# Performance work log

Hardware: AMD Instinct MI355X
Metric: run time of the kernel (lower is better)

The kernel has to match this reference:

```python
import jax, jax.numpy as jnp
import numpy as np

HID = 1024
HEADS = 16

def setup_inputs() -> dict:
    key = jax.random.key(0)
    ks = jax.random.split(key, 9)
    s = 1.0 / np.sqrt(HID)
    x = jax.random.normal(ks[0], (4, 2048, HID), dtype=jnp.float32)
    Wq = jax.random.normal(ks[1], (HID, HID), dtype=jnp.float32) * s
    bq = jnp.zeros((HID,), dtype=jnp.float32)
    Wk = jax.random.normal(ks[2], (HID, HID), dtype=jnp.float32) * s
    bk = jnp.zeros((HID,), dtype=jnp.float32)
    Wv = jax.random.normal(ks[3], (HID, HID), dtype=jnp.float32) * s
    bv = jnp.zeros((HID,), dtype=jnp.float32)
    Wo = jax.random.normal(ks[4], (HID, HID), dtype=jnp.float32) * s
    bo = jnp.zeros((HID,), dtype=jnp.float32)
    return {"x": x, "Wq": Wq, "bq": bq, "Wk": Wk, "bk": bk,
            "Wv": Wv, "bv": bv, "Wo": Wo, "bo": bo}

def _split_heads(t):  # [b, n, hid] -> [b, h, n, d]
    b, n, _ = t.shape
    return t.reshape(b, n, HEADS, HID // HEADS).transpose(0, 2, 1, 3)

def reference(x, Wq, bq, Wk, bk, Wv, bv, Wo, bo):
    # nn.Linear: y = x @ W.T + b
    q = _split_heads(x @ Wq.T + bq)
    k = _split_heads(x @ Wk.T + bk)
    v = _split_heads(x @ Wv.T + bv)
    energy = jnp.einsum('bhqd,bhkd->bhqk', q, k)
    scaling = HID ** 0.5  # note: sqrt(hid_channels), NOT sqrt(head_dim)
    att = jax.nn.softmax(energy / scaling, axis=-1)
    out = jnp.einsum('bhqk,bhkd->bhqd', att, v)
    b, h, n, d = out.shape
    out = out.transpose(0, 2, 1, 3).reshape(b, n, h * d)
    return out @ Wo.T + bo
```

## Files before the change

### kernel.cpp

```cpp
#include <hip/hip_runtime.h>
#include <stdint.h>


#define HID 1024
#define NH 16
#define HD 64
#define BB 4
#define SEQ 2048
#define MTOT (BB * SEQ)

typedef short bf16x8 __attribute__((ext_vector_type(8)));
typedef float f32x4 __attribute__((ext_vector_type(4)));
typedef float f32x16 __attribute__((ext_vector_type(16)));

#define SWZ(row, cb) ((cb) ^ (((row) & 7) << 4))

#define GLDS(gp, lp) __builtin_amdgcn_global_load_lds( \
    (const __attribute__((address_space(1))) void*)(gp), \
    (__attribute__((address_space(3))) void*)(lp), 16, 0, 0)

static __device__ __forceinline__ unsigned short f2bf(float f) {
  unsigned u = __float_as_uint(f);
  u += 0x7fffu + ((u >> 16) & 1u);
  return (unsigned short)(u >> 16);
}

static __device__ __forceinline__ f32x4 mfma16(bf16x8 a, bf16x8 b, f32x4 c) {
  return __builtin_amdgcn_mfma_f32_16x16x32_bf16(a, b, c, 0, 0, 0);
}
static __device__ __forceinline__ f32x16 mfma32(bf16x8 a, bf16x8 b, f32x16 c) {
  return __builtin_amdgcn_mfma_f32_32x32x16_bf16(a, b, c, 0, 0, 0);
}

__global__ void k_cvt_all(const float* __restrict__ x,
                          const float* __restrict__ Wq, const float* __restrict__ Wk,
                          const float* __restrict__ Wv, const float* __restrict__ Wo,
                          unsigned short* __restrict__ ws) {
  const int X4 = MTOT * HID / 4;
  const int W4 = HID * HID / 4;
  int i = blockIdx.x * blockDim.x + threadIdx.x;
  const float* src;
  unsigned short* dst;
  int off;
  if (i < X4) {
    src = x; dst = ws; off = i;
  } else {
    int j = i - X4;
    int w = j / W4;
    off = j - w * W4;
    src = (w == 0) ? Wq : (w == 1) ? Wk : (w == 2) ? Wv : Wo;
    dst = ws + (size_t)MTOT * HID + (size_t)w * HID * HID;
  }
  float4 v = reinterpret_cast<const float4*>(src)[off];
  ushort4 o;
  o.x = f2bf(v.x); o.y = f2bf(v.y); o.z = f2bf(v.z); o.w = f2bf(v.w);
  reinterpret_cast<ushort4*>(dst)[off] = o;
}

__global__ __launch_bounds__(256, 2) void k_gemm3(
    const unsigned short* __restrict__ A,
    const unsigned short* __restrict__ W3,
    const float* __restrict__ bq, const float* __restrict__ bk,
    const float* __restrict__ bv,
    unsigned short* __restrict__ Qo,
    unsigned short* __restrict__ Ko,
    unsigned short* __restrict__ Vto,
    float cexp) {
  const int K = HID;
  __shared__ __align__(16) unsigned short sA[128 * 64];
  __shared__ __align__(16) unsigned short sB[128 * 64];
  const int orig = blockIdx.x + gridDim.x * blockIdx.y;
  const int xcd = orig & 7, idx = orig >> 3;
  const int gm = xcd & 3, gn = xcd >> 1 >> 1;
  const int m0 = (gm * 16 + (idx & 15)) * 128;
  const int n0 = (gn * 12 + (idx >> 4)) * 128;
  const int tid = threadIdx.x;
  const int lane = tid & 63, wid = tid >> 6;
  const int wr = wid >> 1, wc = wid & 1;
  const int lr = lane & 15, lg = lane >> 4;

  f32x4 acc[4][4] = {};

  const unsigned short* gA = A + (size_t)m0 * K;
  const unsigned short* gW = W3 + (size_t)n0 * K;

  for (int kt = 0; kt < K; kt += 64) {
#pragma unroll
    for (int i = 0; i < 4; ++i) {
      int c = tid + i * 256;
      int row = c >> 3, col = (c & 7) << 3;
      GLDS(gA + (size_t)row * K + kt + col, (char*)sA + (size_t)c * 16);
      GLDS(gW + (size_t)row * K + kt + col, (char*)sB + (size_t)c * 16);
    }
    __syncthreads();
#pragma unroll
    for (int kk = 0; kk < 64; kk += 32) {
      bf16x8 a[4], b[4];
      const int co = kk + lg * 8;
#pragma unroll
      for (int m = 0; m < 4; ++m)
        a[m] = *reinterpret_cast<const bf16x8*>(sA + (wr * 64 + m * 16 + lr) * 64 + co);
#pragma unroll
      for (int n = 0; n < 4; ++n)
        b[n] = *reinterpret_cast<const bf16x8*>(sB + (wc * 64 + n * 16 + lr) * 64 + co);
      __builtin_amdgcn_s_setprio(1);
#pragma unroll
      for (int m = 0; m < 4; ++m)
#pragma unroll
        for (int n = 0; n < 4; ++n)
          acc[m][n] = mfma16(a[m], b[n], acc[m][n]);
      __builtin_amdgcn_s_setprio(0);
    }
    __syncthreads();
  }

  const int sect = n0 >> 10;
  const float* bias = (sect == 0) ? bq : (sect == 1) ? bk : bv;
  const float sc = (sect == 0) ? cexp : 1.0f;

  if (sect < 2) {
    unsigned short* C = (sect == 0) ? Qo : Ko;
#pragma unroll
    for (int m = 0; m < 4; ++m) {
      int row0 = m0 + wr * 64 + m * 16 + lg * 4;
      int b = row0 >> 11;
#pragma unroll
      for (int n = 0; n < 4; ++n) {
        int colq = (n0 + wc * 64 + n * 16 + lr) & 1023;
        float bvv = bias[colq];
        int h = colq >> 6, d = colq & 63;
        size_t base = ((size_t)(b * NH + h) * SEQ) * HD + d;
#pragma unroll
        for (int r = 0; r < 4; ++r) {
          int tok = (row0 + r) & 2047;
          C[base + (size_t)tok * HD] = f2bf((acc[m][n][r] + bvv) * sc);
        }
      }
    }
  } else {
#pragma unroll
    for (int m = 0; m < 4; ++m) {
      int row0 = m0 + wr * 64 + m * 16 + lg * 4;
      int b = row0 >> 11;
      int tok0 = row0 & 2047;
#pragma unroll
      for (int n = 0; n < 4; ++n) {
        int colq = (n0 + wc * 64 + n * 16 + lr) & 1023;
        float bvv = bias[colq];
        int h = colq >> 6, d = colq & 63;
        ushort4 pk;
        pk.x = f2bf(acc[m][n][0] + bvv);
        pk.y = f2bf(acc[m][n][1] + bvv);
        pk.z = f2bf(acc[m][n][2] + bvv);
        pk.w = f2bf(acc[m][n][3] + bvv);
        *reinterpret_cast<ushort4*>(&Vto[((size_t)(b * NH + h) * HD + d) * SEQ + tok0]) = pk;
      }
    }
  }
}

__global__ __launch_bounds__(256, 2) void k_gemmo(
    const unsigned short* __restrict__ A,
    const unsigned short* __restrict__ W,
    const float* __restrict__ bias,
    float* __restrict__ C) {
  const int K = HID;
  __shared__ __align__(16) unsigned short sA[128 * 64];
  __shared__ __align__(16) unsigned short sB[128 * 64];
  const int orig = blockIdx.x + gridDim.x * blockIdx.y;
  const int xcd = orig & 7, idx = orig >> 3;
  const int gm = xcd & 3, gn = xcd >> 2;
  const int m0 = (gm * 16 + (idx & 15)) * 128;
  const int n0 = (gn * 4 + (idx >> 4)) * 128;
  const int tid = threadIdx.x;
  const int lane = tid & 63, wid = tid >> 6;
  const int wr = wid >> 1, wc = wid & 1;
  const int lr = lane & 15, lg = lane >> 4;

  f32x4 acc[4][4] = {};

  const unsigned short* gA = A + (size_t)m0 * K;
  const unsigned short* gW = W + (size_t)n0 * K;

  for (int kt = 0; kt < K; kt += 64) {
#pragma unroll
    for (int i = 0; i < 4; ++i) {
      int c = tid + i * 256;
      int row = c >> 3, col = (c & 7) << 3;
      GLDS(gA + (size_t)row * K + kt + col, (char*)sA + (size_t)c * 16);
      GLDS(gW + (size_t)row * K + kt + col, (char*)sB + (size_t)c * 16);
    }
    __syncthreads();
#pragma unroll
    for (int kk = 0; kk < 64; kk += 32) {
      bf16x8 a[4], b[4];
      const int co = kk + lg * 8;
#pragma unroll
      for (int m = 0; m < 4; ++m)
        a[m] = *reinterpret_cast<const bf16x8*>(sA + (wr * 64 + m * 16 + lr) * 64 + co);
#pragma unroll
      for (int n = 0; n < 4; ++n)
        b[n] = *reinterpret_cast<const bf16x8*>(sB + (wc * 64 + n * 16 + lr) * 64 + co);
      __builtin_amdgcn_s_setprio(1);
#pragma unroll
      for (int m = 0; m < 4; ++m)
#pragma unroll
        for (int n = 0; n < 4; ++n)
          acc[m][n] = mfma16(a[m], b[n], acc[m][n]);
      __builtin_amdgcn_s_setprio(0);
    }
    __syncthreads();
  }

#pragma unroll
  for (int m = 0; m < 4; ++m) {
    int row0 = m0 + wr * 64 + m * 16 + lg * 4;
#pragma unroll
    for (int n = 0; n < 4; ++n) {
      int col = n0 + wc * 64 + n * 16 + lr;
      float bvv = bias[col];
#pragma unroll
      for (int r = 0; r < 4; ++r)
        C[(size_t)(row0 + r) * HID + col] = acc[m][n][r] + bvv;
    }
  }
}

#define KVB 64

__global__ __launch_bounds__(256, 4) void k_attn(
    const unsigned short* __restrict__ Qg,
    const unsigned short* __restrict__ Kg,
    const unsigned short* __restrict__ Vt,
    unsigned short* __restrict__ Og) {
  __shared__ __align__(16) unsigned short smem[128 * 64];

  const int bh = blockIdx.x;
  const int qt = blockIdx.y;
  const int tid = threadIdx.x;
  const int lane = tid & 63, wid = tid >> 6;
  const int l31 = lane & 31, hi = lane >> 5;

  const unsigned short* Qh = Qg + ((size_t)bh * SEQ + (size_t)qt * 128) * HD;
  const unsigned short* Kh = Kg + (size_t)bh * SEQ * HD;
  const unsigned short* Vh = Vt + (size_t)bh * HD * SEQ;

  char* sK = (char*)smem;
  char* sV = (char*)smem + 8192;

  const int r0 = tid >> 3, r1 = r0 + 32;
  const int cb0 = SWZ(r0, (tid & 7) << 4) >> 1;
  const int cb1 = SWZ(r1, (tid & 7) << 4) >> 1;

#pragma unroll
  for (int i = 0; i < 4; ++i) {
    int c = tid + i * 256;
    int row = c >> 3;
    int cbl = SWZ(row, (c & 7) << 4);
    GLDS(Qh + (size_t)row * HD + (cbl >> 1), (char*)smem + (size_t)c * 16);
  }
  __syncthreads();
  bf16x8 qb[4];
  {
    int row = wid * 32 + l31;
#pragma unroll
    for (int ks = 0; ks < 4; ++ks)
      qb[ks] = *reinterpret_cast<const bf16x8*>(
          (const char*)smem + row * 128 + SWZ(row, ks * 32 + hi * 16));
  }
  __syncthreads();

  const unsigned short onev = (unsigned short)0x3F80;
  const bf16x8 ones = {(short)onev, (short)onev, (short)onev, (short)onev,
                       (short)onev, (short)onev, (short)onev, (short)onev};

  f32x16 acco[2] = {};
  f32x16 accd = {};

  for (int kt = 0; kt < SEQ; kt += KVB) {
    GLDS(Kh + (size_t)(kt + r0) * HD + cb0, sK + (size_t)tid * 16);
    GLDS(Kh + (size_t)(kt + r1) * HD + cb1, sK + (size_t)(tid + 256) * 16);
    GLDS(Vh + (size_t)r0 * SEQ + kt + cb0, sV + (size_t)tid * 16);
    GLDS(Vh + (size_t)r1 * SEQ + kt + cb1, sV + (size_t)(tid + 256) * 16);
    __syncthreads();

    f32x16 accs[2] = {};
#pragma unroll
    for (int ks = 0; ks < 4; ++ks) {
      bf16x8 ka0 = *reinterpret_cast<const bf16x8*>(
          sK + (0 + l31) * 128 + SWZ(l31, ks * 32 + hi * 16));
      bf16x8 ka1 = *reinterpret_cast<const bf16x8*>(
          sK + (32 + l31) * 128 + SWZ(32 + l31, ks * 32 + hi * 16));
      __builtin_amdgcn_s_setprio(1);
      accs[0] = mfma32(ka0, qb[ks], accs[0]);
      accs[1] = mfma32(ka1, qb[ks], accs[1]);
      __builtin_amdgcn_s_setprio(0);
    }

    bf16x8 pa[4];
#pragma unroll
    for (int nblk = 0; nblk < 2; ++nblk) {
      float p[16];
#pragma unroll
      for (int r = 0; r < 16; ++r) p[r] = exp2f(accs[nblk][r]);
#pragma unroll
      for (int g = 0; g < 2; ++g) {
        const int bs = g * 8;
        unsigned w0, w1, w2, w3;
        asm("v_cvt_pk_bf16_f32 %0, %1, %2" : "=v"(w0) : "v"(p[bs + 0]), "v"(p[bs + 1]));
        asm("v_cvt_pk_bf16_f32 %0, %1, %2" : "=v"(w1) : "v"(p[bs + 2]), "v"(p[bs + 3]));
        asm("v_cvt_pk_bf16_f32 %0, %1, %2" : "=v"(w2) : "v"(p[bs + 4]), "v"(p[bs + 5]));
        asm("v_cvt_pk_bf16_f32 %0, %1, %2" : "=v"(w3) : "v"(p[bs + 6]), "v"(p[bs + 7]));
        uint4 pk4; pk4.x = w0; pk4.y = w1; pk4.z = w2; pk4.w = w3;
        pa[nblk * 2 + g] = *reinterpret_cast<bf16x8*>(&pk4);
      }
    }

#pragma unroll
    for (int i = 0; i < 4; ++i) {
      const int bb = i * 32 + hi * 8;
      bf16x8 vb[2];
#pragma unroll
      for (int dblk = 0; dblk < 2; ++dblk) {
        const int rsw = dblk * 32 + l31;
        const char* rowp = sV + rsw * 128;
        uint2 lo = *reinterpret_cast<const uint2*>(rowp + SWZ(rsw, bb));
        uint2 hi2 = *reinterpret_cast<const uint2*>(rowp + SWZ(rsw, bb + 16));
        uint4 q4; q4.x = lo.x; q4.y = lo.y; q4.z = hi2.x; q4.w = hi2.y;
        vb[dblk] = *reinterpret_cast<bf16x8*>(&q4);
      }
      __builtin_amdgcn_s_setprio(1);
      acco[0] = mfma32(pa[i], vb[0], acco[0]);
      acco[1] = mfma32(pa[i], vb[1], acco[1]);
      accd = mfma32(pa[i], ones, accd);
      __builtin_amdgcn_s_setprio(0);
    }
    __syncthreads();
  }

  const int b = bh >> 4, h = bh & 15;
#pragma unroll
  for (int reg = 0; reg < 16; ++reg) {
    int q = (reg & 3) + 8 * (reg >> 2) + 4 * hi;
    int tok = qt * 128 + wid * 32 + q;
    float rd = 1.0f / accd[reg];
    size_t rowoff = (size_t)(b * SEQ + tok) * HID + h * 64;
    Og[rowoff + l31] = f2bf(acco[0][reg] * rd);
    Og[rowoff + 32 + l31] = f2bf(acco[1][reg] * rd);
  }
}

extern "C" void kernel_launch(void* const* d_in, const int* in_sizes, int n_in,
                              void* d_out, int out_size, void* d_ws, size_t ws_size,
                              hipStream_t stream) {
  (void)in_sizes; (void)n_in; (void)out_size; (void)ws_size;
  const float* x = (const float*)d_in[0];
  const float* Wq = (const float*)d_in[1];
  const float* bq = (const float*)d_in[2];
  const float* Wk = (const float*)d_in[3];
  const float* bk = (const float*)d_in[4];
  const float* Wv = (const float*)d_in[5];
  const float* bv = (const float*)d_in[6];
  const float* Wo = (const float*)d_in[7];
  const float* bo = (const float*)d_in[8];

  unsigned short* ws = (unsigned short*)d_ws;
  unsigned short* xb = ws;
  unsigned short* wqb = xb + (size_t)MTOT * HID;
  unsigned short* wob = wqb + 3 * (size_t)HID * HID;
  unsigned short* qb = wob + (size_t)HID * HID;
  unsigned short* kb = qb + (size_t)MTOT * HID;
  unsigned short* vtb = kb + (size_t)MTOT * HID;
  unsigned short* ob = vtb + (size_t)MTOT * HID;

  const float cexp = 0.04508422f;

  k_cvt_all<<<(MTOT * HID / 4 + 4 * (HID * HID / 4)) / 256, 256, 0, stream>>>(
      x, Wq, Wk, Wv, Wo, ws);

  k_gemm3<<<dim3(64, 24), 256, 0, stream>>>(
      xb, wqb, bq, bk, bv, qb, kb, vtb, cexp);

  k_attn<<<dim3(64, SEQ / 128), 256, 0, stream>>>(qb, kb, vtb, ob);

  k_gemmo<<<dim3(64, 8), 256, 0, stream>>>(ob, wob, bo, (float*)d_out);
}
```

Measured before the change: 211.7 us.

## Prefetch next K/V tiles mid-iteration and load Q directly to registers

The attention loop is restructured so the next K tile is issued right after the QK^T MFMAs and the next V tile right after the PV MFMAs. The asynchronous LDS fills then overlap with the softmax/PV and QK phases instead of stalling at the top of each iteration. Q fragments are now read straight from global memory into registers, which drops the LDS staging pass and one barrier. The cost is reliance on barrier placement for correctness, and the Q reads are per-lane 16-byte global loads that may coalesce less well.

```diff
diff --git a/kernel.cpp b/kernel.cpp
--- a/kernel.cpp
+++ b/kernel.cpp
@@ -227,6 +227,7 @@
 }
 
 #define KVB 64
+#define NT (SEQ / KVB)
 
 __global__ __launch_bounds__(256, 4) void k_attn(
     const unsigned short* __restrict__ Qg,
@@ -241,7 +242,6 @@
   const int lane = tid & 63, wid = tid >> 6;
   const int l31 = lane & 31, hi = lane >> 5;
 
-  const unsigned short* Qh = Qg + ((size_t)bh * SEQ + (size_t)qt * 128) * HD;
   const unsigned short* Kh = Kg + (size_t)bh * SEQ * HD;
   const unsigned short* Vh = Vt + (size_t)bh * HD * SEQ;
 
@@ -252,22 +252,19 @@
   const int cb0 = SWZ(r0, (tid & 7) << 4) >> 1;
   const int cb1 = SWZ(r1, (tid & 7) << 4) >> 1;
 
-#pragma unroll
-  for (int i = 0; i < 4; ++i) {
-    int c = tid + i * 256;
-    int row = c >> 3;
-    int cbl = SWZ(row, (c & 7) << 4);
-    GLDS(Qh + (size_t)row * HD + (cbl >> 1), (char*)smem + (size_t)c * 16);
-  }
-  __syncthreads();
   bf16x8 qb[4];
   {
-    int row = wid * 32 + l31;
+    const unsigned short* Qrow =
+        Qg + ((size_t)bh * SEQ + (size_t)qt * 128 + wid * 32 + l31) * HD;
 #pragma unroll
     for (int ks = 0; ks < 4; ++ks)
-      qb[ks] = *reinterpret_cast<const bf16x8*>(
-          (const char*)smem + row * 128 + SWZ(row, ks * 32 + hi * 16));
-  }
+      qb[ks] = *reinterpret_cast<const bf16x8*>(Qrow + ks * 16 + hi * 8);
+  }
+
+  GLDS(Kh + (size_t)r0 * HD + cb0, sK + (size_t)tid * 16);
+  GLDS(Kh + (size_t)r1 * HD + cb1, sK + (size_t)(tid + 256) * 16);
+  GLDS(Vh + (size_t)r0 * SEQ + cb0, sV + (size_t)tid * 16);
+  GLDS(Vh + (size_t)r1 * SEQ + cb1, sV + (size_t)(tid + 256) * 16);
   __syncthreads();
 
   const unsigned short onev = (unsigned short)0x3F80;
@@ -277,12 +274,9 @@
   f32x16 acco[2] = {};
   f32x16 accd = {};
 
-  for (int kt = 0; kt < SEQ; kt += KVB) {
-    GLDS(Kh + (size_t)(kt + r0) * HD + cb0, sK + (size_t)tid * 16);
-    GLDS(Kh + (size_t)(kt + r1) * HD + cb1, sK + (size_t)(tid + 256) * 16);
-    GLDS(Vh + (size_t)r0 * SEQ + kt + cb0, sV + (size_t)tid * 16);
-    GLDS(Vh + (size_t)r1 * SEQ + kt + cb1, sV + (size_t)(tid + 256) * 16);
-    __syncthreads();
+  for (int t = 0; t < NT; ++t) {
+    const bool pf = (t + 1 < NT);
+    const int ktn = (t + 1) * KVB;
 
     f32x16 accs[2] = {};
 #pragma unroll
@@ -295,6 +289,12 @@
       accs[0] = mfma32(ka0, qb[ks], accs[0]);
       accs[1] = mfma32(ka1, qb[ks], accs[1]);
       __builtin_amdgcn_s_setprio(0);
+    }
+
+    __syncthreads();
+    if (pf) {
+      GLDS(Kh + (size_t)(ktn + r0) * HD + cb0, sK + (size_t)tid * 16);
+      GLDS(Kh + (size_t)(ktn + r1) * HD + cb1, sK + (size_t)(tid + 256) * 16);
     }
 
     bf16x8 pa[4];
@@ -335,7 +335,12 @@
       accd = mfma32(pa[i], ones, accd);
       __builtin_amdgcn_s_setprio(0);
     }
-    __syncthreads();
+
+    __syncthreads();
+    if (pf) {
+      GLDS(Vh + (size_t)r0 * SEQ + ktn + cb0, sV + (size_t)tid * 16);
+      GLDS(Vh + (size_t)r1 * SEQ + ktn + cb1, sV + (size_t)(tid + 256) * 16);
+    }
   }
 
   const int b = bh >> 4, h = bh & 15;
```

Result: no change. 212.4 us (+0.3%).
